# Optimization experiments

Hardware: AMD Instinct MI355X
Metric: run time of the kernel (lower is better)

The kernel has to match this reference:

```python
import jax, jax.numpy as jnp
import numpy as np

NUM_HEADS = 16
HEAD_DIM = 64  # d_out // num_heads


def setup_inputs() -> dict:
    key = jax.random.key(0)
    ks = jax.random.split(key, 6)
    d_in, d_out, b, t = 1024, 1024, 2, 2048
    s = 0.02
    return {
        "x": jax.random.normal(ks[0], (b, t, d_in), jnp.float32),
        "Wq": jax.random.normal(ks[1], (d_in, d_out), jnp.float32) * s,
        "Wk": jax.random.normal(ks[2], (d_in, d_out), jnp.float32) * s,
        "Wv": jax.random.normal(ks[3], (d_in, d_out), jnp.float32) * s,
        "Wo": jax.random.normal(ks[4], (d_out, d_out), jnp.float32) * s,
        "bo": jnp.zeros((d_out,), jnp.float32),
    }


def reference(x, Wq, Wk, Wv, Wo, bo):
    b, t, _ = x.shape
    H, hd = NUM_HEADS, HEAD_DIM
    # qkv projections (no bias), split into heads: [b, H, t, hd]
    q = (x @ Wq).reshape(b, t, H, hd).transpose(0, 2, 1, 3)
    k = (x @ Wk).reshape(b, t, H, hd).transpose(0, 2, 1, 3)
    v = (x @ Wv).reshape(b, t, H, hd).transpose(0, 2, 1, 3)
    # raw scores, causal mask (masked_fill with -1e9 BEFORE the 1/sqrt(hd) scale,
    # matching the source exactly), then scaled softmax
    scores = jnp.einsum("bhqd,bhkd->bhqk", q, k)
    causal = jnp.triu(jnp.ones((t, t), dtype=bool), k=1)
    scores = jnp.where(causal[None, None], jnp.float32(-1e9), scores)
    attn = jax.nn.softmax(scores / jnp.sqrt(jnp.float32(hd)), axis=-1)
    # dropout is identity in eval mode
    ctx = jnp.einsum("bhqk,bhkd->bhqd", attn, v)  # [b, H, t, hd]
    ctx = ctx.transpose(0, 2, 1, 3).reshape(b, t, H * hd)
    return ctx @ Wo + bo
```

## Files before the change

kernel.cpp:

```cpp
#include <hip/hip_runtime.h>


#define SEQ   2048
#define DMODEL 1024
#define NH    16
#define HD    64
#define MROWS 4096

typedef __attribute__((ext_vector_type(4))) float f32x4;
typedef __attribute__((ext_vector_type(16))) float f32x16;
typedef __attribute__((ext_vector_type(8))) short short8;
typedef __attribute__((ext_vector_type(4))) unsigned int u32x4;

#define MFMA16(a, b, c) __builtin_amdgcn_mfma_f32_16x16x32_bf16((a), (b), (c), 0, 0, 0)
#define MFMA32(a, b, c) __builtin_amdgcn_mfma_f32_32x32x16_bf16((a), (b), (c), 0, 0, 0)

__device__ __forceinline__ unsigned short f2bf(float f) {
  union { float f; unsigned u; } v; v.f = f;
  return (unsigned short)((v.u + 0x7fffu + ((v.u >> 16) & 1u)) >> 16);
}

__device__ __forceinline__ float exp2x(float x) {
#if __has_builtin(__builtin_amdgcn_exp2f)
  return __builtin_amdgcn_exp2f(x);
#else
  float r; asm("v_exp_f32 %0, %1" : "=v"(r) : "v"(x)); return r;
#endif
}

__device__ __forceinline__ unsigned cvt_pk(float lo, float hi) {
  unsigned r;
  asm volatile("v_cvt_pk_bf16_f32 %0, %1, %2" : "=v"(r) : "v"(lo), "v"(hi));
  return r;
}

__device__ __forceinline__ void pls(unsigned& a, unsigned& b) {
  asm("v_permlane32_swap_b32 %0, %1" : "+v"(a), "+v"(b));
}

__device__ __forceinline__ short8 as_short8(u32x4 v) {
  union { u32x4 u; short8 s; } x; x.u = v; return x.s;
}

__device__ __forceinline__ f32x4 zero4() {
  f32x4 z; z[0] = 0.f; z[1] = 0.f; z[2] = 0.f; z[3] = 0.f; return z;
}

__device__ __forceinline__ void async16(const void* g, void* l) {
  __builtin_amdgcn_global_load_lds(
      (const __attribute__((address_space(1))) unsigned int*)g,
      (__attribute__((address_space(3))) unsigned int*)l, 16, 0, 0);
}

__global__ __launch_bounds__(256) void prep(
    const float* __restrict__ x, const float* __restrict__ Wq,
    const float* __restrict__ Wk, const float* __restrict__ Wv,
    const float* __restrict__ Wo, unsigned short* __restrict__ xb,
    unsigned short* __restrict__ Wt, unsigned short* __restrict__ WoT) {
  __shared__ unsigned short tile[64][65];
  const int bx = blockIdx.x;
  if (bx < 2048) {
    int i = bx * 256 + threadIdx.x;
    const float4* p = (const float4*)x;
    float4 a = p[2 * i];
    float4 b = p[2 * i + 1];
    short8 o;
    o[0] = (short)f2bf(a.x); o[1] = (short)f2bf(a.y);
    o[2] = (short)f2bf(a.z); o[3] = (short)f2bf(a.w);
    o[4] = (short)f2bf(b.x); o[5] = (short)f2bf(b.y);
    o[6] = (short)f2bf(b.z); o[7] = (short)f2bf(b.w);
    *(short8*)&xb[(size_t)i * 8] = o;
    return;
  }
  const int id2 = bx - 2048;
  const int m = id2 >> 8;
  const float* W = (m == 0) ? Wq : (m == 1) ? Wk : (m == 2) ? Wv : Wo;
  unsigned short* D = (m == 3) ? WoT : Wt + (size_t)m * 1024 * 1024;
  const int tid = id2 & 255;
  const int kb = (tid >> 4) * 64, nb = (tid & 15) * 64;
  const int t = threadIdx.x;
  const int tx = t & 63, ty = t >> 6;
#pragma unroll
  for (int rr = 0; rr < 16; rr++) {
    int r = ty * 16 + rr;
    tile[r][tx] = f2bf(W[(size_t)(kb + r) * 1024 + nb + tx]);
  }
  __syncthreads();
#pragma unroll
  for (int rr = 0; rr < 16; rr++) {
    int r = ty * 16 + rr;
    D[(size_t)(nb + r) * 1024 + kb + tx] = tile[tx][r];
  }
}

__global__ __launch_bounds__(256) void vtrans(const unsigned short* __restrict__ V,
                                              unsigned short* __restrict__ Vt) {
  __shared__ unsigned short tile[64][65];
  int t = threadIdx.x;
  int tx = t & 63, ty = t >> 6;
  int bh = blockIdx.x, t0 = blockIdx.y * 64;
  const unsigned short* src = V + ((size_t)bh * SEQ + t0) * HD;
  unsigned short* dst = Vt + (size_t)bh * HD * SEQ + t0;
#pragma unroll
  for (int rr = 0; rr < 16; rr++) {
    int r = ty * 16 + rr;
    tile[r][tx] = src[(size_t)r * HD + tx];
  }
  __syncthreads();
#pragma unroll
  for (int rr = 0; rr < 16; rr++) {
    int r = ty * 16 + rr;
    dst[(size_t)r * SEQ + tx] = tile[tx][r];
  }
}

template <int MODE, int WMF>
__global__ __launch_bounds__(256) void gemm_bt(
    const unsigned short* __restrict__ A, const unsigned short* __restrict__ Bt,
    unsigned short* __restrict__ Qo, unsigned short* __restrict__ Ko,
    unsigned short* __restrict__ Vo, float* __restrict__ out,
    const float* __restrict__ bo) {
  constexpr int K = 1024;
  constexpr int BM = WMF * 32;
  constexpr int NT = K / 32;
  __shared__ __align__(16) unsigned short As[3][BM * 32];
  __shared__ __align__(16) unsigned short Bs[3][128 * 32];
  const int t = threadIdx.x;
  const int lane = t & 63;
  const int w = t >> 6;
  const int lr = lane & 15, kf = lane >> 4;
  const int wr = w >> 1, wc = w & 1;

  const int nwg = gridDim.x * gridDim.y;
  const int id = blockIdx.y * gridDim.x + blockIdx.x;
  const int swz = (id & 7) * (nwg >> 3) + (id >> 3);
  const int bx = swz % gridDim.x, by = swz / gridDim.x;

  const int rowbase = bx * BM;
  const int colbase = by * 128;

  const unsigned short* Ab = A + (size_t)rowbase * K;
  const unsigned short* Bb = Bt + (size_t)colbase * K;

  f32x4 acc[WMF][4];
#pragma unroll
  for (int m = 0; m < WMF; m++)
#pragma unroll
    for (int n = 0; n < 4; n++) acc[m][n] = zero4();

  auto stage = [&](int buf, int kt) {
    int k0 = kt * 32;
#pragma unroll
    for (int i = 0; i < BM / 64; i++) {
      int f = i * 256 + t;
      int c = f ^ ((f >> 3) & 3);
      int row = c >> 2;
      int col = (c & 3) << 3;
      async16(Ab + (size_t)row * K + k0 + col, (char*)&As[buf][0] + (size_t)f * 16);
    }
#pragma unroll
    for (int i = 0; i < 2; i++) {
      int f = i * 256 + t;
      int c = f ^ ((f >> 3) & 3);
      int row = c >> 2;
      int col = (c & 3) << 3;
      async16(Bb + (size_t)row * K + k0 + col, (char*)&Bs[buf][0] + (size_t)f * 16);
    }
  };

  stage(0, 0);
  stage(1, 1);

  for (int kt = 0; kt < NT; kt++) {
    if (kt + 2 < NT) {
      stage((kt + 2) % 3, kt + 2);
      if constexpr (MODE == 0) asm volatile("s_waitcnt vmcnt(8)" ::: "memory");
      else                     asm volatile("s_waitcnt vmcnt(6)" ::: "memory");
    } else if (kt + 1 < NT) {
      if constexpr (MODE == 0) asm volatile("s_waitcnt vmcnt(4)" ::: "memory");
      else                     asm volatile("s_waitcnt vmcnt(3)" ::: "memory");
    } else {
      asm volatile("s_waitcnt vmcnt(0)" ::: "memory");
    }
    __builtin_amdgcn_s_barrier();

    const int cur = kt % 3;
    short8 av[WMF], bv[4];
#pragma unroll
    for (int m = 0; m < WMF; m++) {
      int row = wr * (WMF * 16) + m * 16 + lr;
      int idx = (row * 32 + kf * 8) ^ (((row >> 1) & 3) << 3);
      av[m] = *(const short8*)&As[cur][idx];
    }
#pragma unroll
    for (int n = 0; n < 4; n++) {
      int row = wc * 64 + n * 16 + lr;
      int idx = (row * 32 + kf * 8) ^ (((row >> 1) & 3) << 3);
      bv[n] = *(const short8*)&Bs[cur][idx];
    }
    __builtin_amdgcn_s_setprio(1);
#pragma unroll
    for (int m = 0; m < WMF; m++)
#pragma unroll
      for (int n = 0; n < 4; n++) acc[m][n] = MFMA16(av[m], bv[n], acc[m][n]);
    __builtin_amdgcn_s_setprio(0);
    __builtin_amdgcn_s_barrier();
  }

  if constexpr (MODE == 0) {
#pragma unroll
    for (int n = 0; n < 4; n++) {
      int c = colbase + wc * 64 + n * 16 + lr;
      int sel = c >> 10;
      int hh = (c >> 6) & 15;
      int dd = c & 63;
      unsigned short* dst = (sel == 0) ? Qo : ((sel == 1) ? Ko : Vo);
      const float sc = (sel == 0) ? 0.18033688011112042f : 1.0f;
#pragma unroll
      for (int m = 0; m < WMF; m++) {
        int r0 = rowbase + wr * (WMF * 16) + m * 16 + kf * 4;
#pragma unroll
        for (int i = 0; i < 4; i++) {
          int r = r0 + i;
          int bi = r >> 11;
          int tq = r & 2047;
          size_t off = ((size_t)(bi * NH + hh) * SEQ + tq) * HD + dd;
          dst[off] = f2bf(acc[m][n][i] * sc);
        }
      }
    }
  } else {
#pragma unroll
    for (int n = 0; n < 4; n++) {
      int c = colbase + wc * 64 + n * 16 + lr;
      float bias = bo[c];
#pragma unroll
      for (int m = 0; m < WMF; m++) {
        int r0 = rowbase + wr * (WMF * 16) + m * 16 + kf * 4;
#pragma unroll
        for (int i = 0; i < 4; i++) {
          out[(size_t)(r0 + i) * 1024 + c] = acc[m][n][i] + bias;
        }
      }
    }
  }
}

__global__ __launch_bounds__(256) void attn_fwd(
    const unsigned short* __restrict__ Q, const unsigned short* __restrict__ K,
    const unsigned short* __restrict__ Vt, unsigned short* __restrict__ ctx) {
  const int bh = blockIdx.x;
  const int y = blockIdx.y;
  const int qt = (y < 8) ? (15 - y) : (y - 8);
  const int bi = bh >> 4, hh = bh & 15;
  const int t = threadIdx.x, lane = t & 63, w = t >> 6;
  const int qc = lane & 31, hi = lane >> 5;

  __shared__ __align__(16) unsigned short Ks[2][64 * 64];
  __shared__ __align__(16) unsigned short Vs[2][64 * 64];

  const unsigned short* Qb = Q + (size_t)bh * SEQ * HD;
  const unsigned short* Kb = K + (size_t)bh * SEQ * HD;
  const unsigned short* Vb = Vt + (size_t)bh * HD * SEQ;

  const int qrow = qt * 128 + w * 32;
  short8 qv[4];
#pragma unroll
  for (int c = 0; c < 4; c++)
    qv[c] = *(const short8*)&Qb[(size_t)(qrow + qc) * HD + c * 16 + hi * 8];

  f32x16 o0, o1;
#pragma unroll
  for (int i = 0; i < 16; i++) { o0[i] = 0.f; o1[i] = 0.f; }
  float l_acc = 0.f;

  const int ktmax = 2 * qt + (w >> 1);
  const int KT = 2 * qt + 2;

  auto stage = [&](int buf, int kt) {
#pragma unroll
    for (int i2 = 0; i2 < 2; i2++) {
      int f = i2 * 256 + t;
      int c = f ^ ((f >> 3) & 7);
      async16(Kb + (size_t)kt * 64 * HD + (size_t)c * 8,
              (char*)&Ks[buf][0] + (size_t)f * 16);
      int d = c >> 3, ko = (c & 7) << 3;
      async16(Vb + (size_t)d * SEQ + (size_t)kt * 64 + ko,
              (char*)&Vs[buf][0] + (size_t)f * 16);
    }
  };

  auto tile = [&](const unsigned short* Kt, const unsigned short* Vtile, int kt) {
    f32x16 s0, s1;
#pragma unroll
    for (int i = 0; i < 16; i++) { s0[i] = 0.f; s1[i] = 0.f; }
    __builtin_amdgcn_s_setprio(1);
#pragma unroll
    for (int c = 0; c < 4; c++) {
      int i0 = (qc * 64 + c * 16 + hi * 8) ^ ((qc & 7) << 3);
      s0 = MFMA32(*(const short8*)&Kt[i0], qv[c], s0);
      int r1 = 32 + qc;
      int i1 = (r1 * 64 + c * 16 + hi * 8) ^ ((r1 & 7) << 3);
      s1 = MFMA32(*(const short8*)&Kt[i1], qv[c], s1);
    }
    __builtin_amdgcn_s_setprio(0);

    if (kt == ktmax) {
      const int qg = qrow + qc;
#pragma unroll
      for (int reg = 0; reg < 16; reg++) {
        int rloc = (reg & 3) + 8 * (reg >> 2) + 4 * hi;
        int kg = kt * 64 + rloc;
        if (kg > qg) s0[reg] = -1e30f;
        if (kg + 32 > qg) s1[reg] = -1e30f;
      }
    }

    unsigned w0[8], w1[8];
    float psA = 0.f, psB = 0.f;
#pragma unroll
    for (int j = 0; j < 8; j++) {
      float a0 = exp2x(s0[2 * j]), b0 = exp2x(s0[2 * j + 1]);
      float a1 = exp2x(s1[2 * j]), b1 = exp2x(s1[2 * j + 1]);
      psA += a0 + b0;
      psB += a1 + b1;
      w0[j] = cvt_pk(a0, b0);
      w1[j] = cvt_pk(a1, b1);
    }
    l_acc += psA + psB;

    __builtin_amdgcn_s_setprio(1);
#pragma unroll
    for (int h2 = 0; h2 < 2; h2++) {
      unsigned* pw = h2 ? w1 : w0;
#pragma unroll
      for (int cc = 0; cc < 2; cc++) {
        unsigned a0 = pw[cc * 4 + 0], b0 = pw[cc * 4 + 2];
        unsigned a1 = pw[cc * 4 + 1], b1 = pw[cc * 4 + 3];
        pls(a0, b0);
        pls(a1, b1);
        u32x4 pf; pf[0] = a0; pf[1] = a1; pf[2] = b0; pf[3] = b1;
        short8 pfrag = as_short8(pf);
        int c2 = h2 * 2 + cc;
        int ia = (qc * 64 + c2 * 16 + hi * 8) ^ ((qc & 7) << 3);
        o0 = MFMA32(*(const short8*)&Vtile[ia], pfrag, o0);
        int rb = 32 + qc;
        int ib = (rb * 64 + c2 * 16 + hi * 8) ^ ((rb & 7) << 3);
        o1 = MFMA32(*(const short8*)&Vtile[ib], pfrag, o1);
      }
    }
    __builtin_amdgcn_s_setprio(0);
  };

  stage(0, 0);
  int cur = 0;

  for (int kt = 0; kt < KT; kt++) {
    if (kt + 1 < KT) {
      stage(cur ^ 1, kt + 1);
      asm volatile("s_waitcnt vmcnt(4)" ::: "memory");
    } else {
      asm volatile("s_waitcnt vmcnt(0)" ::: "memory");
    }
    __builtin_amdgcn_s_barrier();

    if (kt <= ktmax) tile(&Ks[cur][0], &Vs[cur][0], kt);

    __builtin_amdgcn_s_barrier();
    cur ^= 1;
  }

  float l = l_acc + __shfl_xor(l_acc, 32);
  float inv = 1.0f / l;
  const size_t rowoff = ((size_t)bi * SEQ + qrow + qc) * DMODEL + hh * HD;
#pragma unroll
  for (int g = 0; g < 4; g++) {
    unsigned pa = cvt_pk(o0[4 * g] * inv, o0[4 * g + 1] * inv);
    unsigned pb = cvt_pk(o0[4 * g + 2] * inv, o0[4 * g + 3] * inv);
    uint2 vv; vv.x = pa; vv.y = pb;
    *(uint2*)&ctx[rowoff + 8 * g + 4 * hi] = vv;
    unsigned pc = cvt_pk(o1[4 * g] * inv, o1[4 * g + 1] * inv);
    unsigned pd = cvt_pk(o1[4 * g + 2] * inv, o1[4 * g + 3] * inv);
    uint2 ww; ww.x = pc; ww.y = pd;
    *(uint2*)&ctx[rowoff + 32 + 8 * g + 4 * hi] = ww;
  }
}

extern "C" void kernel_launch(void* const* d_in, const int* in_sizes, int n_in,
                              void* d_out, int out_size, void* d_ws, size_t ws_size,
                              hipStream_t stream) {
  const float* x  = (const float*)d_in[0];
  const float* Wq = (const float*)d_in[1];
  const float* Wk = (const float*)d_in[2];
  const float* Wv = (const float*)d_in[3];
  const float* Wo = (const float*)d_in[4];
  const float* bo = (const float*)d_in[5];
  float* out = (float*)d_out;

  unsigned short* xb   = (unsigned short*)d_ws;
  unsigned short* Wt   = xb + (size_t)MROWS * DMODEL;
  unsigned short* WoT  = Wt + (size_t)3 * 1024 * 1024;
  unsigned short* Qb   = WoT + (size_t)1024 * 1024;
  unsigned short* Kb   = Qb + (size_t)MROWS * DMODEL;
  unsigned short* Vb   = Kb + (size_t)MROWS * DMODEL;
  unsigned short* ctxb = Vb + (size_t)MROWS * DMODEL;

  prep<<<3072, 256, 0, stream>>>(x, Wq, Wk, Wv, Wo, xb, Wt, WoT);

  gemm_bt<0, 4><<<dim3(32, 24), 256, 0, stream>>>(xb, Wt, Qb, Kb, ctxb, nullptr, nullptr);
  vtrans<<<dim3(32, 32), 256, 0, stream>>>(ctxb, Vb);
  attn_fwd<<<dim3(32, 16), 256, 0, stream>>>(Qb, Kb, Vb, ctxb);
  gemm_bt<1, 2><<<dim3(64, 8), 256, 0, stream>>>(ctxb, WoT, nullptr, nullptr, nullptr, out, bo);
}
```

Before: 120.8 us.

## Fuse V transpose into QKV GEMM epilogue and stage two KV tiles per step

The QKV projection GEMM now writes the V output already transposed (head-dim major) through an LDS transpose in its epilogue, which removes the separate vtrans kernel launch and its round trip through global memory. The attention kernel now stages two 64-key tiles per pipeline step, doubling the LDS buffers, halving the number of barriers, and issuing larger prefetch batches. The cost is higher LDS use in attention, which may reduce occupancy, plus an extra syncthreads in the GEMM epilogue.

```diff
diff --git a/kernel.cpp b/kernel.cpp
--- a/kernel.cpp
+++ b/kernel.cpp
@@ -93,27 +93,6 @@
   }
 }
 
-__global__ __launch_bounds__(256) void vtrans(const unsigned short* __restrict__ V,
-                                              unsigned short* __restrict__ Vt) {
-  __shared__ unsigned short tile[64][65];
-  int t = threadIdx.x;
-  int tx = t & 63, ty = t >> 6;
-  int bh = blockIdx.x, t0 = blockIdx.y * 64;
-  const unsigned short* src = V + ((size_t)bh * SEQ + t0) * HD;
-  unsigned short* dst = Vt + (size_t)bh * HD * SEQ + t0;
-#pragma unroll
-  for (int rr = 0; rr < 16; rr++) {
-    int r = ty * 16 + rr;
-    tile[r][tx] = src[(size_t)r * HD + tx];
-  }
-  __syncthreads();
-#pragma unroll
-  for (int rr = 0; rr < 16; rr++) {
-    int r = ty * 16 + rr;
-    dst[(size_t)r * SEQ + tx] = tile[tx][r];
-  }
-}
-
 template <int MODE, int WMF>
 __global__ __launch_bounds__(256) void gemm_bt(
     const unsigned short* __restrict__ A, const unsigned short* __restrict__ Bt,
@@ -123,8 +102,9 @@
   constexpr int K = 1024;
   constexpr int BM = WMF * 32;
   constexpr int NT = K / 32;
-  __shared__ __align__(16) unsigned short As[3][BM * 32];
-  __shared__ __align__(16) unsigned short Bs[3][128 * 32];
+  __shared__ __align__(16) unsigned short smem[3 * BM * 32 + 3 * 128 * 32];
+  unsigned short* Asb = smem;
+  unsigned short* Bsb = smem + 3 * BM * 32;
   const int t = threadIdx.x;
   const int lane = t & 63;
   const int w = t >> 6;
@@ -156,7 +136,8 @@
       int c = f ^ ((f >> 3) & 3);
       int row = c >> 2;
       int col = (c & 3) << 3;
-      async16(Ab + (size_t)row * K + k0 + col, (char*)&As[buf][0] + (size_t)f * 16);
+      async16(Ab + (size_t)row * K + k0 + col,
+              (char*)(Asb + (size_t)buf * BM * 32) + (size_t)f * 16);
     }
 #pragma unroll
     for (int i = 0; i < 2; i++) {
@@ -164,7 +145,8 @@
       int c = f ^ ((f >> 3) & 3);
       int row = c >> 2;
       int col = (c & 3) << 3;
-      async16(Bb + (size_t)row * K + k0 + col, (char*)&Bs[buf][0] + (size_t)f * 16);
+      async16(Bb + (size_t)row * K + k0 + col,
+              (char*)(Bsb + (size_t)buf * 128 * 32) + (size_t)f * 16);
     }
   };
 
@@ -184,19 +166,20 @@
     }
     __builtin_amdgcn_s_barrier();
 
-    const int cur = kt % 3;
+    const unsigned short* As = Asb + (size_t)(kt % 3) * BM * 32;
+    const unsigned short* Bs = Bsb + (size_t)(kt % 3) * 128 * 32;
     short8 av[WMF], bv[4];
 #pragma unroll
     for (int m = 0; m < WMF; m++) {
       int row = wr * (WMF * 16) + m * 16 + lr;
       int idx = (row * 32 + kf * 8) ^ (((row >> 1) & 3) << 3);
-      av[m] = *(const short8*)&As[cur][idx];
+      av[m] = *(const short8*)&As[idx];
     }
 #pragma unroll
     for (int n = 0; n < 4; n++) {
       int row = wc * 64 + n * 16 + lr;
       int idx = (row * 32 + kf * 8) ^ (((row >> 1) & 3) << 3);
-      bv[n] = *(const short8*)&Bs[cur][idx];
+      bv[n] = *(const short8*)&Bs[idx];
     }
     __builtin_amdgcn_s_setprio(1);
 #pragma unroll
@@ -208,25 +191,52 @@
   }
 
   if constexpr (MODE == 0) {
-#pragma unroll
-    for (int n = 0; n < 4; n++) {
-      int c = colbase + wc * 64 + n * 16 + lr;
-      int sel = c >> 10;
-      int hh = (c >> 6) & 15;
-      int dd = c & 63;
-      unsigned short* dst = (sel == 0) ? Qo : ((sel == 1) ? Ko : Vo);
-      const float sc = (sel == 0) ? 0.18033688011112042f : 1.0f;
-#pragma unroll
-      for (int m = 0; m < WMF; m++) {
-        int r0 = rowbase + wr * (WMF * 16) + m * 16 + kf * 4;
-#pragma unroll
-        for (int i = 0; i < 4; i++) {
-          int r = r0 + i;
-          int bi = r >> 11;
-          int tq = r & 2047;
-          size_t off = ((size_t)(bi * NH + hh) * SEQ + tq) * HD + dd;
-          dst[off] = f2bf(acc[m][n][i] * sc);
+    if (colbase < 2048) {
+      const int selq = colbase >> 10;
+      unsigned short* dst = selq ? Ko : Qo;
+      const float sc = selq ? 1.0f : 0.18033688011112042f;
+#pragma unroll
+      for (int n = 0; n < 4; n++) {
+        int c = colbase + wc * 64 + n * 16 + lr;
+        int hh = (c >> 6) & 15;
+        int dd = c & 63;
+#pragma unroll
+        for (int m = 0; m < WMF; m++) {
+          int r0 = rowbase + wr * (WMF * 16) + m * 16 + kf * 4;
+#pragma unroll
+          for (int i = 0; i < 4; i++) {
+            int r = r0 + i;
+            int bi = r >> 11;
+            int tq = r & 2047;
+            dst[((size_t)(bi * NH + hh) * SEQ + tq) * HD + dd] = f2bf(acc[m][n][i] * sc);
+          }
         }
+      }
+    } else {
+      unsigned short* tr = smem;
+#pragma unroll
+      for (int n = 0; n < 4; n++) {
+        int ccol = wc * 64 + n * 16 + lr;
+#pragma unroll
+        for (int m = 0; m < WMF; m++) {
+#pragma unroll
+          for (int i = 0; i < 4; i++) {
+            int rrow = wr * (WMF * 16) + m * 16 + kf * 4 + i;
+            tr[ccol * 136 + rrow] = f2bf(acc[m][n][i]);
+          }
+        }
+      }
+      __syncthreads();
+      const int bi2 = rowbase >> 11;
+      const int tq0 = rowbase & 2047;
+#pragma unroll
+      for (int k2 = 0; k2 < 8; k2++) {
+        int u = k2 * 256 + t;
+        int cc = u >> 4, seg = u & 15;
+        int c = colbase + cc;
+        int hh = (c >> 6) & 15, dd = c & 63;
+        short8 v8 = *(const short8*)&tr[cc * 136 + seg * 8];
+        *(short8*)&Vo[((size_t)(bi2 * NH + hh) * HD + dd) * SEQ + tq0 + seg * 8] = v8;
       }
     }
   } else {
@@ -256,8 +266,8 @@
   const int t = threadIdx.x, lane = t & 63, w = t >> 6;
   const int qc = lane & 31, hi = lane >> 5;
 
-  __shared__ __align__(16) unsigned short Ks[2][64 * 64];
-  __shared__ __align__(16) unsigned short Vs[2][64 * 64];
+  __shared__ __align__(16) unsigned short Ks[2][2][64 * 64];
+  __shared__ __align__(16) unsigned short Vs[2][2][64 * 64];
 
   const unsigned short* Qb = Q + (size_t)bh * SEQ * HD;
   const unsigned short* Kb = K + (size_t)bh * SEQ * HD;
@@ -275,18 +285,22 @@
   float l_acc = 0.f;
 
   const int ktmax = 2 * qt + (w >> 1);
-  const int KT = 2 * qt + 2;
-
-  auto stage = [&](int buf, int kt) {
-#pragma unroll
-    for (int i2 = 0; i2 < 2; i2++) {
-      int f = i2 * 256 + t;
-      int c = f ^ ((f >> 3) & 7);
-      async16(Kb + (size_t)kt * 64 * HD + (size_t)c * 8,
-              (char*)&Ks[buf][0] + (size_t)f * 16);
-      int d = c >> 3, ko = (c & 7) << 3;
-      async16(Vb + (size_t)d * SEQ + (size_t)kt * 64 + ko,
-              (char*)&Vs[buf][0] + (size_t)f * 16);
+  const int NP = qt + 1;
+
+  auto stage = [&](int buf, int p) {
+#pragma unroll
+    for (int sub = 0; sub < 2; sub++) {
+      int kt = 2 * p + sub;
+#pragma unroll
+      for (int i2 = 0; i2 < 2; i2++) {
+        int f = i2 * 256 + t;
+        int c = f ^ ((f >> 3) & 7);
+        async16(Kb + (size_t)kt * 64 * HD + (size_t)c * 8,
+                (char*)&Ks[buf][sub][0] + (size_t)f * 16);
+        int d = c >> 3, ko = (c & 7) << 3;
+        async16(Vb + (size_t)d * SEQ + (size_t)kt * 64 + ko,
+                (char*)&Vs[buf][sub][0] + (size_t)f * 16);
+      }
     }
   };
 
@@ -355,16 +369,17 @@
   stage(0, 0);
   int cur = 0;
 
-  for (int kt = 0; kt < KT; kt++) {
-    if (kt + 1 < KT) {
-      stage(cur ^ 1, kt + 1);
-      asm volatile("s_waitcnt vmcnt(4)" ::: "memory");
+  for (int p = 0; p < NP; p++) {
+    if (p + 1 < NP) {
+      stage(cur ^ 1, p + 1);
+      asm volatile("s_waitcnt vmcnt(8)" ::: "memory");
     } else {
       asm volatile("s_waitcnt vmcnt(0)" ::: "memory");
     }
     __builtin_amdgcn_s_barrier();
 
-    if (kt <= ktmax) tile(&Ks[cur][0], &Vs[cur][0], kt);
+    if (2 * p <= ktmax)     tile(&Ks[cur][0][0], &Vs[cur][0][0], 2 * p);
+    if (2 * p + 1 <= ktmax) tile(&Ks[cur][1][0], &Vs[cur][1][0], 2 * p + 1);
 
     __builtin_amdgcn_s_barrier();
     cur ^= 1;
@@ -407,8 +422,7 @@
 
   prep<<<3072, 256, 0, stream>>>(x, Wq, Wk, Wv, Wo, xb, Wt, WoT);
 
-  gemm_bt<0, 4><<<dim3(32, 24), 256, 0, stream>>>(xb, Wt, Qb, Kb, ctxb, nullptr, nullptr);
-  vtrans<<<dim3(32, 32), 256, 0, stream>>>(ctxb, Vb);
+  gemm_bt<0, 4><<<dim3(32, 24), 256, 0, stream>>>(xb, Wt, Qb, Kb, Vb, nullptr, nullptr);
   attn_fwd<<<dim3(32, 16), 256, 0, stream>>>(Qb, Kb, Vb, ctxb);
   gemm_bt<1, 2><<<dim3(64, 8), 256, 0, stream>>>(ctxb, WoT, nullptr, nullptr, nullptr, out, bo);
 }
```

Measured after the change: 106.2 us. 1.14x faster.
